# Optimization experiments

Hardware: AMD Instinct MI355X
Metric: run time of the kernel (lower is better)

## Reference

```python
import jax, jax.numpy as jnp
import numpy as np

N = 50000
E = 400000
IN_FEATS = 512
HEADS = 8
OUT_FEATS = 64
NEG_SLOPE = 0.2


def setup_inputs() -> dict:
    key = jax.random.key(0)
    ks = jax.random.split(key, 12)
    HF = HEADS * OUT_FEATS
    s = 1.0 / np.sqrt(IN_FEATS)
    inp = {
        "feat": jax.random.normal(ks[0], (N, IN_FEATS), dtype=jnp.float32),
        "src": jax.random.randint(ks[1], (E,), 0, N, dtype=jnp.int32),
        "dst": jax.random.randint(ks[2], (E,), 0, N, dtype=jnp.int32),
        "W_src": jax.random.normal(ks[3], (IN_FEATS, HF), dtype=jnp.float32) * s,
        "b_src": jax.random.normal(ks[4], (HF,), dtype=jnp.float32) * 0.01,
        "W_dst": jax.random.normal(ks[5], (IN_FEATS, HF), dtype=jnp.float32) * s,
        "b_dst": jax.random.normal(ks[6], (HF,), dtype=jnp.float32) * 0.01,
        "W_val": jax.random.normal(ks[7], (IN_FEATS, HF), dtype=jnp.float32) * s,
        "b_val": jax.random.normal(ks[8], (HF,), dtype=jnp.float32) * 0.01,
        "attn_l": jax.random.normal(ks[9], (HEADS, OUT_FEATS), dtype=jnp.float32) * 0.1,
        "attn_r": jax.random.normal(ks[10], (HEADS, OUT_FEATS), dtype=jnp.float32) * 0.1,
    }
    return inp


def reference(feat, src, dst, W_src, b_src, W_dst, b_dst, W_val, b_val, attn_l, attn_r):
    # node projections: [N, H, F]
    feat_src = (feat @ W_src + b_src).reshape(N, HEADS, OUT_FEATS)
    feat_dst = (feat @ W_dst + b_dst).reshape(N, HEADS, OUT_FEATS)
    feat_v = (feat @ W_val + b_val).reshape(N, HEADS, OUT_FEATS)

    # per-node attention logits: [N, H]
    el = jnp.einsum("nhf,hf->nh", feat_src, attn_l)
    er = jnp.einsum("nhf,hf->nh", feat_dst, attn_r)

    # per-edge logits with leaky relu: [E, H]
    e = el[src] + er[dst]
    e = jnp.where(e >= 0, e, NEG_SLOPE * e)

    # edge softmax segmented by destination node
    e_max = jax.ops.segment_max(e, dst, num_segments=N)  # [N, H]
    e_max = jnp.where(jnp.isfinite(e_max), e_max, 0.0)
    exp_e = jnp.exp(e - e_max[dst])  # [E, H]
    denom = jax.ops.segment_sum(exp_e, dst, num_segments=N)  # [N, H]
    a = exp_e / jnp.maximum(denom[dst], 1e-16)  # [E, H]

    # weighted gather-scatter aggregation: [N, H, F]
    msg = feat_v[src] * a[:, :, None]
    rst = jax.ops.segment_sum(msg, dst, num_segments=N)
    return rst.reshape(N, HEADS * OUT_FEATS)
```

## Files before the change

kernel.cpp:

```cpp
#include <hip/hip_runtime.h>
#include <math.h>

constexpr int N_NODES = 50000;
constexpr int N_PAD   = 50048;
constexpr int N_EDGES = 400000;
constexpr int IN_F = 512;
constexpr int HEADS = 8;
constexpr int OUT_F = 64;
constexpr int HF = 512;
constexpr float NEG = 0.2f;

typedef __bf16 bf16x8 __attribute__((ext_vector_type(8)));
typedef float  f32x4  __attribute__((ext_vector_type(4)));

__device__ __forceinline__ unsigned short f2bf(float f) {
    unsigned u = __float_as_uint(f);
    u += 0x7fffu + ((u >> 16) & 1u);
    return (unsigned short)(u >> 16);
}
__device__ __forceinline__ unsigned packbf2(float lo, float hi) {
    return (unsigned)f2bf(lo) | ((unsigned)f2bf(hi) << 16);
}

constexpr int K0_CONV_BLOCKS = 12500;
constexpr int K0_ZERO_BLOCKS = (N_NODES + 255) / 256;

__global__ __launch_bounds__(256) void k0_convert(const float* __restrict__ in,
                                                  unsigned short* __restrict__ out,
                                                  int* __restrict__ deg) {
    int b = blockIdx.x;
    if (b < K0_CONV_BLOCKS) {
        int idx = b * 256 + threadIdx.x;
        size_t base = (size_t)idx * 8;
        float4 a = *(const float4*)(in + base);
        float4 c = *(const float4*)(in + base + 4);
        uint4 v;
        v.x = packbf2(a.x, a.y);
        v.y = packbf2(a.z, a.w);
        v.z = packbf2(c.x, c.y);
        v.w = packbf2(c.z, c.w);
        *(uint4*)(out + base) = v;
    } else {
        int idx = (b - K0_CONV_BLOCKS) * 256 + threadIdx.x;
        if (idx < N_NODES) deg[idx] = 0;
    }
}

constexpr int K14_HIST0 = 289;
constexpr int K14_BLOCKS = K14_HIST0 + (N_EDGES + 255) / 256;

__global__ __launch_bounds__(256) void k14_misc(
        const float* __restrict__ W_val, unsigned short* __restrict__ Wt,
        const float* __restrict__ W_src, const float* __restrict__ b_src,
        const float* __restrict__ W_dst, const float* __restrict__ b_dst,
        const float* __restrict__ attn_l, const float* __restrict__ attn_r,
        float* __restrict__ w_l, float* __restrict__ w_r,
        float* __restrict__ c_l, float* __restrict__ c_r,
        const int* __restrict__ dst, int* __restrict__ deg) {
    __shared__ float tile[32][33];
    int b = blockIdx.x, t = threadIdx.x;
    if (b < 256) {
        int bi = b >> 4, bj = b & 15;
        for (int i = t; i < 1024; i += 256) {
            int r = i >> 5, c = i & 31;
            tile[r][c] = W_val[(size_t)(bi * 32 + r) * HF + bj * 32 + c];
        }
        __syncthreads();
        for (int i = t; i < 1024; i += 256) {
            int r = i >> 5, c = i & 31;
            Wt[(size_t)(bj * 32 + r) * IN_F + bi * 32 + c] = f2bf(tile[c][r]);
        }
    } else if (b < K14_HIST0) {
        int gid = (b - 256) * 256 + t;
        if (gid < 4096) {
            int k = gid >> 3, h = gid & 7;
            float s = 0.f;
            #pragma unroll 8
            for (int f = 0; f < OUT_F; ++f) s += W_src[k * HF + h * OUT_F + f] * attn_l[h * OUT_F + f];
            w_l[k * 8 + h] = s;
        } else if (gid < 8192) {
            int g = gid - 4096;
            int k = g >> 3, h = g & 7;
            float s = 0.f;
            #pragma unroll 8
            for (int f = 0; f < OUT_F; ++f) s += W_dst[k * HF + h * OUT_F + f] * attn_r[h * OUT_F + f];
            w_r[k * 8 + h] = s;
        } else if (gid < 8192 + 16) {
            int g = gid - 8192;
            int h = g & 7;
            float s = 0.f;
            if (g < 8) {
                for (int f = 0; f < OUT_F; ++f) s += b_src[h * OUT_F + f] * attn_l[h * OUT_F + f];
                c_l[h] = s;
            } else {
                for (int f = 0; f < OUT_F; ++f) s += b_dst[h * OUT_F + f] * attn_r[h * OUT_F + f];
                c_r[h] = s;
            }
        }
    } else {
        int e = (b - K14_HIST0) * 256 + t;
        if (e < N_EDGES) atomicAdd(&deg[dst[e]], 1);
    }
}

__global__ __launch_bounds__(256) void k2_el_er(
        const float* __restrict__ feat,
        const float* __restrict__ w_l, const float* __restrict__ w_r,
        const float* __restrict__ c_l, const float* __restrict__ c_r,
        float* __restrict__ el, float* __restrict__ er) {
    __shared__ float swl[4096];
    __shared__ float swr[4096];
    int t = threadIdx.x;
    for (int i = t; i < 4096; i += 256) { swl[i] = w_l[i]; swr[i] = w_r[i]; }
    __syncthreads();

    int node = blockIdx.x * 16 + (t >> 4);
    if (node >= N_NODES) return;
    int sub = t & 15, h = sub & 7, side = sub >> 3;

    const float* w = side ? swr : swl;
    float acc = side ? c_r[h] : c_l[h];
    const float* frow = feat + (size_t)node * IN_F;
    for (int k = 0; k < IN_F; k += 4) {
        float4 f = *(const float4*)(frow + k);
        acc = fmaf(f.x, w[(k + 0) * 8 + h], acc);
        acc = fmaf(f.y, w[(k + 1) * 8 + h], acc);
        acc = fmaf(f.z, w[(k + 2) * 8 + h], acc);
        acc = fmaf(f.w, w[(k + 3) * 8 + h], acc);
    }
    if (side) er[node * 8 + h] = acc; else el[node * 8 + h] = acc;
}

__global__ __launch_bounds__(1024) void kS_scan(const int* __restrict__ deg,
                                                int* __restrict__ offs,
                                                int* __restrict__ cursor) {
    __shared__ int wsum[16];
    __shared__ int base_s;
    int b = blockIdx.x, t = threadIdx.x;
    int lane = t & 63, wid = t >> 6;

    int pre = 0;
    for (int i = t; i < b * 1024; i += 1024) pre += deg[i];
    #pragma unroll
    for (int off = 32; off; off >>= 1) pre += __shfl_down(pre, (unsigned)off, 64);
    if (lane == 0) wsum[wid] = pre;
    __syncthreads();
    if (t == 0) {
        int s = 0;
        for (int i = 0; i < 16; ++i) s += wsum[i];
        base_s = s;
    }
    __syncthreads();
    int base = base_s;
    __syncthreads();

    int i = b * 1024 + t;
    int v = (i < N_NODES) ? deg[i] : 0;
    int x = v;
    #pragma unroll
    for (int off = 1; off < 64; off <<= 1) {
        int y = __shfl_up(x, (unsigned)off, 64);
        if (lane >= off) x += y;
    }
    if (lane == 63) wsum[wid] = x;
    __syncthreads();
    if (wid == 0) {
        int s = (lane < 16) ? wsum[lane] : 0;
        #pragma unroll
        for (int off = 1; off < 16; off <<= 1) {
            int y = __shfl_up(s, (unsigned)off, 64);
            if (lane >= off) s += y;
        }
        if (lane < 16) wsum[lane] = s;
    }
    __syncthreads();
    int woff = wid ? wsum[wid - 1] : 0;
    if (i < N_NODES) {
        int excl = base + woff + x - v;
        offs[i] = excl;
        cursor[i] = excl;
    }
}

__global__ __launch_bounds__(256) void k3_mfma(
        const unsigned short* __restrict__ Abf,
        const unsigned short* __restrict__ Bbf,
        const float* __restrict__ bias,
        unsigned short* __restrict__ C) {
    __shared__ unsigned short As[128 * 64];
    __shared__ unsigned short Bs[128 * 64];
    int tid = threadIdx.x;
    int w = tid >> 6, lane = tid & 63;
    int bm = blockIdx.x >> 2, bn = blockIdx.x & 3;
    int rowBase = bm * 128, colBase = bn * 128;
    int wm = w >> 1, wn = w & 1;
    int c15 = lane & 15, q = lane >> 4;

    f32x4 acc[4][4] = {};

    for (int k0 = 0; k0 < IN_F; k0 += 64) {
        #pragma unroll
        for (int rnd = 0; rnd < 4; ++rnd) {
            int e = w * 256 + rnd * 64 + lane;
            int r = e >> 3, p = e & 7;
            int lc = p ^ (r & 7);
            const unsigned short* gA = Abf + (size_t)(rowBase + r) * IN_F + k0 + lc * 8;
            unsigned short* lA = &As[(w * 256 + rnd * 64) * 8];
            __builtin_amdgcn_global_load_lds(
                (const __attribute__((address_space(1))) unsigned int*)gA,
                (__attribute__((address_space(3))) unsigned int*)lA, 16, 0, 0);
            const unsigned short* gB = Bbf + (size_t)(colBase + r) * IN_F + k0 + lc * 8;
            unsigned short* lB = &Bs[(w * 256 + rnd * 64) * 8];
            __builtin_amdgcn_global_load_lds(
                (const __attribute__((address_space(1))) unsigned int*)gB,
                (__attribute__((address_space(3))) unsigned int*)lB, 16, 0, 0);
        }
        __syncthreads();

        #pragma unroll
        for (int ks = 0; ks < 2; ++ks) {
            bf16x8 a[4], b[4];
            #pragma unroll
            for (int mi = 0; mi < 4; ++mi) {
                int row = wm * 64 + mi * 16 + c15;
                int pc = (ks * 4 + q) ^ (row & 7);
                a[mi] = *(const bf16x8*)&As[row * 64 + pc * 8];
            }
            #pragma unroll
            for (int nj = 0; nj < 4; ++nj) {
                int row = wn * 64 + nj * 16 + c15;
                int pc = (ks * 4 + q) ^ (row & 7);
                b[nj] = *(const bf16x8*)&Bs[row * 64 + pc * 8];
            }
            #pragma unroll
            for (int mi = 0; mi < 4; ++mi)
                #pragma unroll
                for (int nj = 0; nj < 4; ++nj)
                    acc[mi][nj] = __builtin_amdgcn_mfma_f32_16x16x32_bf16(
                        a[mi], b[nj], acc[mi][nj], 0, 0, 0);
        }
        __syncthreads();
    }

    #pragma unroll
    for (int nj = 0; nj < 4; ++nj) {
        int col = colBase + wn * 64 + nj * 16 + c15;
        float bv = bias[col];
        #pragma unroll
        for (int mi = 0; mi < 4; ++mi) {
            int row0 = rowBase + wm * 64 + mi * 16 + q * 4;
            #pragma unroll
            for (int rg = 0; rg < 4; ++rg) {
                C[(size_t)(row0 + rg) * HF + col] = f2bf(acc[mi][nj][rg] + bv);
            }
        }
    }
}

__global__ __launch_bounds__(256) void k6_scatter(
        const int* __restrict__ src, const int* __restrict__ dst,
        int* __restrict__ cursor, int* __restrict__ srcs) {
    int e = blockIdx.x * 256 + threadIdx.x;
    if (e < N_EDGES) {
        int pos = atomicAdd(&cursor[dst[e]], 1);
        srcs[pos] = src[e];
    }
}

__device__ __forceinline__ void accum8(float* acc, uint4 v, float w) {
    unsigned u;
    u = v.x;
    acc[0] = fmaf(w, __uint_as_float(u << 16), acc[0]);
    acc[1] = fmaf(w, __uint_as_float(u & 0xffff0000u), acc[1]);
    u = v.y;
    acc[2] = fmaf(w, __uint_as_float(u << 16), acc[2]);
    acc[3] = fmaf(w, __uint_as_float(u & 0xffff0000u), acc[3]);
    u = v.z;
    acc[4] = fmaf(w, __uint_as_float(u << 16), acc[4]);
    acc[5] = fmaf(w, __uint_as_float(u & 0xffff0000u), acc[5]);
    u = v.w;
    acc[6] = fmaf(w, __uint_as_float(u << 16), acc[6]);
    acc[7] = fmaf(w, __uint_as_float(u & 0xffff0000u), acc[7]);
}

__global__ __launch_bounds__(256) void k8_agg(
        const int* __restrict__ srcs, const int* __restrict__ offs,
        const int* __restrict__ deg,
        const float* __restrict__ el, const float* __restrict__ er,
        const uint4* __restrict__ feat_v,
        float* __restrict__ out) {
    int lane = threadIdx.x & 63;
    int n = blockIdx.x * 4 + (threadIdx.x >> 6);
    int start = offs[n], cnt = deg[n];
    int h = lane >> 3;
    float erh = er[(size_t)n * 8 + h];
    float acc[8] = {};
    float dsum = 0.f;

    for (int base = 0; base < cnt; base += 64) {
        int m = cnt - base; if (m > 64) m = 64;
        int s_all = (lane < m) ? srcs[start + base + lane] : 0;
        int i = 0;
        for (; i + 8 <= m; i += 8) {
            int s[8]; uint4 v[8]; float e[8];
            #pragma unroll
            for (int j = 0; j < 8; ++j) s[j] = __shfl(s_all, i + j, 64);
            #pragma unroll
            for (int j = 0; j < 8; ++j) v[j] = feat_v[(size_t)s[j] * 64 + lane];
            #pragma unroll
            for (int j = 0; j < 8; ++j) e[j] = el[(size_t)s[j] * 8 + h];
            #pragma unroll
            for (int j = 0; j < 8; ++j) {
                float x = e[j] + erh;
                x = (x >= 0.f) ? x : NEG * x;
                float w = __expf(x);
                dsum += w;
                accum8(acc, v[j], w);
            }
        }
        for (; i < m; ++i) {
            int s0 = __shfl(s_all, i, 64);
            uint4 v0 = feat_v[(size_t)s0 * 64 + lane];
            float x = el[(size_t)s0 * 8 + h] + erh;
            x = (x >= 0.f) ? x : NEG * x;
            float w = __expf(x);
            dsum += w;
            accum8(acc, v0, w);
        }
    }

    float dn = 1.f / fmaxf(dsum, 1e-16f);
    float* op = out + (size_t)n * HF + lane * 8;
    *(float4*)op       = make_float4(acc[0] * dn, acc[1] * dn, acc[2] * dn, acc[3] * dn);
    *(float4*)(op + 4) = make_float4(acc[4] * dn, acc[5] * dn, acc[6] * dn, acc[7] * dn);
}

extern "C" void kernel_launch(void* const* d_in, const int* in_sizes, int n_in,
                              void* d_out, int out_size, void* d_ws, size_t ws_size,
                              hipStream_t stream) {
    const float* feat   = (const float*)d_in[0];
    const int*   src    = (const int*)d_in[1];
    const int*   dst    = (const int*)d_in[2];
    const float* W_src  = (const float*)d_in[3];
    const float* b_src  = (const float*)d_in[4];
    const float* W_dst  = (const float*)d_in[5];
    const float* b_dst  = (const float*)d_in[6];
    const float* W_val  = (const float*)d_in[7];
    const float* b_val  = (const float*)d_in[8];
    const float* attn_l = (const float*)d_in[9];
    const float* attn_r = (const float*)d_in[10];
    float* out = (float*)d_out;

    char* ws = (char*)d_ws;
    size_t off = 0;
    auto alloc = [&](size_t bytes) -> void* {
        void* p = ws + off;
        off += (bytes + 255) & ~(size_t)255;
        return p;
    };

    unsigned short* feat_bf = (unsigned short*)alloc((size_t)N_PAD * IN_F * 2);
    unsigned short* Wt      = (unsigned short*)alloc((size_t)IN_F * HF * 2);
    unsigned short* feat_v  = (unsigned short*)alloc((size_t)N_PAD * HF * 2);
    float* w_l    = (float*)alloc(4096 * 4);
    float* w_r    = (float*)alloc(4096 * 4);
    float* c_l    = (float*)alloc(8 * 4);
    float* c_r    = (float*)alloc(8 * 4);
    float* el     = (float*)alloc((size_t)N_NODES * 8 * 4);
    float* er     = (float*)alloc((size_t)N_NODES * 8 * 4);
    int*   deg    = (int*)alloc((size_t)N_NODES * 4);
    int*   offs   = (int*)alloc((size_t)N_NODES * 4);
    int*   cursor = (int*)alloc((size_t)N_NODES * 4);
    int*   srcs   = (int*)alloc((size_t)N_EDGES * 4);
    (void)ws_size; (void)in_sizes; (void)n_in; (void)out_size;

    k0_convert<<<K0_CONV_BLOCKS + K0_ZERO_BLOCKS, 256, 0, stream>>>(feat, feat_bf, deg);
    k14_misc<<<K14_BLOCKS, 256, 0, stream>>>(W_val, Wt, W_src, b_src, W_dst, b_dst,
                                             attn_l, attn_r, w_l, w_r, c_l, c_r, dst, deg);
    k2_el_er<<<(N_NODES + 15) / 16, 256, 0, stream>>>(feat, w_l, w_r, c_l, c_r, el, er);
    kS_scan<<<(N_NODES + 1023) / 1024, 1024, 0, stream>>>(deg, offs, cursor);
    k3_mfma<<<(N_PAD / 128) * 4, 256, 0, stream>>>(feat_bf, Wt, b_val, feat_v);
    k6_scatter<<<(N_EDGES + 255) / 256, 256, 0, stream>>>(src, dst, cursor, srcs);
    k8_agg<<<N_NODES / 4, 256, 0, stream>>>(srcs, offs, deg, el, er,
                                            (const uint4*)feat_v, out);
}
```

Before: 422.9 us.

## Fuse bf16 feature conversion with el/er projection in persistent kernel

Merges the fp32-to-bf16 conversion of feat and the per-node el/er logit projection into one persistent kernel, so feat (about 100 MB) is read once instead of twice. Each wave handles one row, keeps its slice of the folded attention weights in registers, prefetches the next row, and reduces the 16 outputs with a transpose-style shuffle butterfly. Degree zeroing moves to hipMemsetAsync. The cost is heavy register use from 32 float4 weight registers, and a fixed grid of 1024 blocks.

```diff
diff --git a/kernel.cpp b/kernel.cpp
--- a/kernel.cpp
+++ b/kernel.cpp
@@ -20,30 +20,6 @@
 }
 __device__ __forceinline__ unsigned packbf2(float lo, float hi) {
     return (unsigned)f2bf(lo) | ((unsigned)f2bf(hi) << 16);
-}
-
-constexpr int K0_CONV_BLOCKS = 12500;
-constexpr int K0_ZERO_BLOCKS = (N_NODES + 255) / 256;
-
-__global__ __launch_bounds__(256) void k0_convert(const float* __restrict__ in,
-                                                  unsigned short* __restrict__ out,
-                                                  int* __restrict__ deg) {
-    int b = blockIdx.x;
-    if (b < K0_CONV_BLOCKS) {
-        int idx = b * 256 + threadIdx.x;
-        size_t base = (size_t)idx * 8;
-        float4 a = *(const float4*)(in + base);
-        float4 c = *(const float4*)(in + base + 4);
-        uint4 v;
-        v.x = packbf2(a.x, a.y);
-        v.y = packbf2(a.z, a.w);
-        v.z = packbf2(c.x, c.y);
-        v.w = packbf2(c.z, c.w);
-        *(uint4*)(out + base) = v;
-    } else {
-        int idx = (b - K0_CONV_BLOCKS) * 256 + threadIdx.x;
-        if (idx < N_NODES) deg[idx] = 0;
-    }
 }
 
 constexpr int K14_HIST0 = 289;
@@ -103,32 +79,137 @@
     }
 }
 
-__global__ __launch_bounds__(256) void k2_el_er(
+constexpr int K0F_GRID = 1024;
+
+__global__ __launch_bounds__(256, 2) void k0_fused(
         const float* __restrict__ feat,
         const float* __restrict__ w_l, const float* __restrict__ w_r,
         const float* __restrict__ c_l, const float* __restrict__ c_r,
+        unsigned short* __restrict__ feat_bf,
         float* __restrict__ el, float* __restrict__ er) {
-    __shared__ float swl[4096];
-    __shared__ float swr[4096];
+    __shared__ float4 lw[2048];
     int t = threadIdx.x;
-    for (int i = t; i < 4096; i += 256) { swl[i] = w_l[i]; swr[i] = w_r[i]; }
-    __syncthreads();
-
-    int node = blockIdx.x * 16 + (t >> 4);
-    if (node >= N_NODES) return;
-    int sub = t & 15, h = sub & 7, side = sub >> 3;
-
-    const float* w = side ? swr : swl;
-    float acc = side ? c_r[h] : c_l[h];
-    const float* frow = feat + (size_t)node * IN_F;
-    for (int k = 0; k < IN_F; k += 4) {
-        float4 f = *(const float4*)(frow + k);
-        acc = fmaf(f.x, w[(k + 0) * 8 + h], acc);
-        acc = fmaf(f.y, w[(k + 1) * 8 + h], acc);
-        acc = fmaf(f.z, w[(k + 2) * 8 + h], acc);
-        acc = fmaf(f.w, w[(k + 3) * 8 + h], acc);
-    }
-    if (side) er[node * 8 + h] = acc; else el[node * 8 + h] = acc;
+    int lane = t & 63, wv = t >> 6;
+
+    const float4* gl = (const float4*)w_l;
+    const float4* gr = (const float4*)w_r;
+    #pragma unroll
+    for (int p = 0; p < 8; ++p) {
+        int i = t + 256 * p;
+        int sw = i ^ ((i >> 4) & 7);
+        lw[sw] = (i < 1024) ? gl[i] : gr[i - 1024];
+    }
+    __syncthreads();
+
+    float4 wl0[8], wl1[8], wr0[8], wr1[8];
+    #pragma unroll
+    for (int j = 0; j < 8; ++j) {
+        int i0 = 16 * lane + 2 * j;
+        wl0[j] = lw[i0 ^ ((i0 >> 4) & 7)];
+        int i1 = i0 + 1;
+        wl1[j] = lw[i1 ^ ((i1 >> 4) & 7)];
+        int i2 = 1024 + i0;
+        wr0[j] = lw[i2 ^ ((i2 >> 4) & 7)];
+        int i3 = i2 + 1;
+        wr1[j] = lw[i3 ^ ((i3 >> 4) & 7)];
+    }
+
+    int idx = ((lane & 1) << 3) | ((lane & 2) << 1) | ((lane & 4) >> 1) | ((lane & 8) >> 3);
+    int oh = idx & 7, oside = idx >> 3;
+    float cadd = 0.f;
+    if (lane < 16) cadd = oside ? c_r[oh] : c_l[oh];
+
+    const int NQ = N_NODES / 4;
+    int q = blockIdx.x;
+    if (q >= NQ) return;
+
+    float4 f0, f1;
+    {
+        const float* fr = feat + (size_t)(q * 4 + wv) * IN_F + lane * 8;
+        f0 = *(const float4*)fr;
+        f1 = *(const float4*)(fr + 4);
+    }
+
+    while (true) {
+        int qn = q + K0F_GRID;
+        float4 n0, n1;
+        if (qn < NQ) {
+            const float* fr = feat + (size_t)(qn * 4 + wv) * IN_F + lane * 8;
+            n0 = *(const float4*)fr;
+            n1 = *(const float4*)(fr + 4);
+        }
+
+        int row = q * 4 + wv;
+        uint4 vv;
+        vv.x = packbf2(f0.x, f0.y); vv.y = packbf2(f0.z, f0.w);
+        vv.z = packbf2(f1.x, f1.y); vv.w = packbf2(f1.z, f1.w);
+        *(uint4*)(feat_bf + (size_t)row * IN_F + lane * 8) = vv;
+
+        float v[16];
+        #pragma unroll
+        for (int c = 0; c < 16; ++c) v[c] = 0.f;
+        float ff[8] = {f0.x, f0.y, f0.z, f0.w, f1.x, f1.y, f1.z, f1.w};
+        #pragma unroll
+        for (int j = 0; j < 8; ++j) {
+            float f = ff[j];
+            v[0]  = fmaf(f, wl0[j].x, v[0]);
+            v[1]  = fmaf(f, wl0[j].y, v[1]);
+            v[2]  = fmaf(f, wl0[j].z, v[2]);
+            v[3]  = fmaf(f, wl0[j].w, v[3]);
+            v[4]  = fmaf(f, wl1[j].x, v[4]);
+            v[5]  = fmaf(f, wl1[j].y, v[5]);
+            v[6]  = fmaf(f, wl1[j].z, v[6]);
+            v[7]  = fmaf(f, wl1[j].w, v[7]);
+            v[8]  = fmaf(f, wr0[j].x, v[8]);
+            v[9]  = fmaf(f, wr0[j].y, v[9]);
+            v[10] = fmaf(f, wr0[j].z, v[10]);
+            v[11] = fmaf(f, wr0[j].w, v[11]);
+            v[12] = fmaf(f, wr1[j].x, v[12]);
+            v[13] = fmaf(f, wr1[j].y, v[13]);
+            v[14] = fmaf(f, wr1[j].z, v[14]);
+            v[15] = fmaf(f, wr1[j].w, v[15]);
+        }
+
+        #pragma unroll
+        for (int j = 0; j < 8; ++j) {
+            float a = v[j], b = v[j + 8];
+            float send = (lane & 1) ? a : b;
+            float recv = __shfl_xor(send, 1, 64);
+            v[j] = ((lane & 1) ? b : a) + recv;
+        }
+        #pragma unroll
+        for (int j = 0; j < 4; ++j) {
+            float a = v[j], b = v[j + 4];
+            float send = (lane & 2) ? a : b;
+            float recv = __shfl_xor(send, 2, 64);
+            v[j] = ((lane & 2) ? b : a) + recv;
+        }
+        #pragma unroll
+        for (int j = 0; j < 2; ++j) {
+            float a = v[j], b = v[j + 2];
+            float send = (lane & 4) ? a : b;
+            float recv = __shfl_xor(send, 4, 64);
+            v[j] = ((lane & 4) ? b : a) + recv;
+        }
+        {
+            float a = v[0], b = v[1];
+            float send = (lane & 8) ? a : b;
+            float recv = __shfl_xor(send, 8, 64);
+            v[0] = ((lane & 8) ? b : a) + recv;
+        }
+        float tot = v[0];
+        tot += __shfl_xor(tot, 16, 64);
+        tot += __shfl_xor(tot, 32, 64);
+
+        if (lane < 16) {
+            float o = tot + cadd;
+            if (oside) er[(size_t)row * 8 + oh] = o;
+            else       el[(size_t)row * 8 + oh] = o;
+        }
+
+        if (qn >= NQ) break;
+        q = qn; f0 = n0; f1 = n1;
+    }
 }
 
 __global__ __launch_bounds__(1024) void kS_scan(const int* __restrict__ deg,
@@ -374,10 +455,10 @@
     int*   srcs   = (int*)alloc((size_t)N_EDGES * 4);
     (void)ws_size; (void)in_sizes; (void)n_in; (void)out_size;
 
-    k0_convert<<<K0_CONV_BLOCKS + K0_ZERO_BLOCKS, 256, 0, stream>>>(feat, feat_bf, deg);
+    hipMemsetAsync(deg, 0, (size_t)N_NODES * 4, stream);
     k14_misc<<<K14_BLOCKS, 256, 0, stream>>>(W_val, Wt, W_src, b_src, W_dst, b_dst,
                                              attn_l, attn_r, w_l, w_r, c_l, c_r, dst, deg);
-    k2_el_er<<<(N_NODES + 15) / 16, 256, 0, stream>>>(feat, w_l, w_r, c_l, c_r, el, er);
+    k0_fused<<<K0F_GRID, 256, 0, stream>>>(feat, w_l, w_r, c_l, c_r, feat_bf, el, er);
     kS_scan<<<(N_NODES + 1023) / 1024, 1024, 0, stream>>>(deg, offs, cursor);
     k3_mfma<<<(N_PAD / 128) * 4, 256, 0, stream>>>(feat_bf, Wt, b_val, feat_v);
     k6_scatter<<<(N_EDGES + 255) / 256, 256, 0, stream>>>(src, dst, cursor, srcs);
```

Result: faster. 377.5 us (-10.7%).

## Fuse fp32-to-bf16 conversion and el/er logits into the MFMA projection GEMM

Applied to the files above, without the earlier changes.

Removes the separate feature conversion kernel and the el/er dot-product kernel. The GEMM now loads fp32 features directly, converts them to bf16 into LDS, and computes the 16 per-node attention logits with extra MFMAs against a bf16 folded weight matrix in one column-block. This avoids writing and re-reading a bf16 copy of feat and a second full pass over feat. In exchange, A-tile loads become synchronous register loads instead of async global-to-LDS loads, and the logits are now computed in bf16 precision rather than fp32.

```diff
diff --git a/kernel.cpp b/kernel.cpp
--- a/kernel.cpp
+++ b/kernel.cpp
@@ -22,30 +22,6 @@
     return (unsigned)f2bf(lo) | ((unsigned)f2bf(hi) << 16);
 }
 
-constexpr int K0_CONV_BLOCKS = 12500;
-constexpr int K0_ZERO_BLOCKS = (N_NODES + 255) / 256;
-
-__global__ __launch_bounds__(256) void k0_convert(const float* __restrict__ in,
-                                                  unsigned short* __restrict__ out,
-                                                  int* __restrict__ deg) {
-    int b = blockIdx.x;
-    if (b < K0_CONV_BLOCKS) {
-        int idx = b * 256 + threadIdx.x;
-        size_t base = (size_t)idx * 8;
-        float4 a = *(const float4*)(in + base);
-        float4 c = *(const float4*)(in + base + 4);
-        uint4 v;
-        v.x = packbf2(a.x, a.y);
-        v.y = packbf2(a.z, a.w);
-        v.z = packbf2(c.x, c.y);
-        v.w = packbf2(c.z, c.w);
-        *(uint4*)(out + base) = v;
-    } else {
-        int idx = (b - K0_CONV_BLOCKS) * 256 + threadIdx.x;
-        if (idx < N_NODES) deg[idx] = 0;
-    }
-}
-
 constexpr int K14_HIST0 = 289;
 constexpr int K14_BLOCKS = K14_HIST0 + (N_EDGES + 255) / 256;
 
@@ -54,8 +30,7 @@
         const float* __restrict__ W_src, const float* __restrict__ b_src,
         const float* __restrict__ W_dst, const float* __restrict__ b_dst,
         const float* __restrict__ attn_l, const float* __restrict__ attn_r,
-        float* __restrict__ w_l, float* __restrict__ w_r,
-        float* __restrict__ c_l, float* __restrict__ c_r,
+        unsigned short* __restrict__ w_lr, float* __restrict__ c_lr,
         const int* __restrict__ dst, int* __restrict__ deg) {
     __shared__ float tile[32][33];
     int b = blockIdx.x, t = threadIdx.x;
@@ -77,58 +52,30 @@
             float s = 0.f;
             #pragma unroll 8
             for (int f = 0; f < OUT_F; ++f) s += W_src[k * HF + h * OUT_F + f] * attn_l[h * OUT_F + f];
-            w_l[k * 8 + h] = s;
+            w_lr[h * IN_F + k] = f2bf(s);
         } else if (gid < 8192) {
             int g = gid - 4096;
             int k = g >> 3, h = g & 7;
             float s = 0.f;
             #pragma unroll 8
             for (int f = 0; f < OUT_F; ++f) s += W_dst[k * HF + h * OUT_F + f] * attn_r[h * OUT_F + f];
-            w_r[k * 8 + h] = s;
+            w_lr[(8 + h) * IN_F + k] = f2bf(s);
         } else if (gid < 8192 + 16) {
             int g = gid - 8192;
             int h = g & 7;
             float s = 0.f;
             if (g < 8) {
                 for (int f = 0; f < OUT_F; ++f) s += b_src[h * OUT_F + f] * attn_l[h * OUT_F + f];
-                c_l[h] = s;
+                c_lr[h] = s;
             } else {
                 for (int f = 0; f < OUT_F; ++f) s += b_dst[h * OUT_F + f] * attn_r[h * OUT_F + f];
-                c_r[h] = s;
+                c_lr[8 + h] = s;
             }
         }
     } else {
         int e = (b - K14_HIST0) * 256 + t;
         if (e < N_EDGES) atomicAdd(&deg[dst[e]], 1);
     }
-}
-
-__global__ __launch_bounds__(256) void k2_el_er(
-        const float* __restrict__ feat,
-        const float* __restrict__ w_l, const float* __restrict__ w_r,
-        const float* __restrict__ c_l, const float* __restrict__ c_r,
-        float* __restrict__ el, float* __restrict__ er) {
-    __shared__ float swl[4096];
-    __shared__ float swr[4096];
-    int t = threadIdx.x;
-    for (int i = t; i < 4096; i += 256) { swl[i] = w_l[i]; swr[i] = w_r[i]; }
-    __syncthreads();
-
-    int node = blockIdx.x * 16 + (t >> 4);
-    if (node >= N_NODES) return;
-    int sub = t & 15, h = sub & 7, side = sub >> 3;
-
-    const float* w = side ? swr : swl;
-    float acc = side ? c_r[h] : c_l[h];
-    const float* frow = feat + (size_t)node * IN_F;
-    for (int k = 0; k < IN_F; k += 4) {
-        float4 f = *(const float4*)(frow + k);
-        acc = fmaf(f.x, w[(k + 0) * 8 + h], acc);
-        acc = fmaf(f.y, w[(k + 1) * 8 + h], acc);
-        acc = fmaf(f.z, w[(k + 2) * 8 + h], acc);
-        acc = fmaf(f.w, w[(k + 3) * 8 + h], acc);
-    }
-    if (side) er[node * 8 + h] = acc; else el[node * 8 + h] = acc;
 }
 
 __global__ __launch_bounds__(1024) void kS_scan(const int* __restrict__ deg,
@@ -182,11 +129,16 @@
     }
 }
 
-__global__ __launch_bounds__(256) void k3_mfma(
-        const unsigned short* __restrict__ Abf,
+constexpr int K3_GRID = (N_PAD / 128) * 4;
+
+__global__ __launch_bounds__(256) void k3_fused(
+        const float* __restrict__ feat,
         const unsigned short* __restrict__ Bbf,
+        const unsigned short* __restrict__ w_lr,
+        const float* __restrict__ c_lr,
         const float* __restrict__ bias,
-        unsigned short* __restrict__ C) {
+        unsigned short* __restrict__ C,
+        float* __restrict__ el, float* __restrict__ er) {
     __shared__ unsigned short As[128 * 64];
     __shared__ unsigned short Bs[128 * 64];
     int tid = threadIdx.x;
@@ -195,8 +147,10 @@
     int rowBase = bm * 128, colBase = bn * 128;
     int wm = w >> 1, wn = w & 1;
     int c15 = lane & 15, q = lane >> 4;
+    bool doE = (bn == 0) && (wn == 0);
 
     f32x4 acc[4][4] = {};
+    f32x4 accE[4] = {};
 
     for (int k0 = 0; k0 < IN_F; k0 += 64) {
         #pragma unroll
@@ -204,16 +158,26 @@
             int e = w * 256 + rnd * 64 + lane;
             int r = e >> 3, p = e & 7;
             int lc = p ^ (r & 7);
-            const unsigned short* gA = Abf + (size_t)(rowBase + r) * IN_F + k0 + lc * 8;
-            unsigned short* lA = &As[(w * 256 + rnd * 64) * 8];
-            __builtin_amdgcn_global_load_lds(
-                (const __attribute__((address_space(1))) unsigned int*)gA,
-                (__attribute__((address_space(3))) unsigned int*)lA, 16, 0, 0);
             const unsigned short* gB = Bbf + (size_t)(colBase + r) * IN_F + k0 + lc * 8;
-            unsigned short* lB = &Bs[(w * 256 + rnd * 64) * 8];
+            unsigned short* lB = &Bs[e * 8];
             __builtin_amdgcn_global_load_lds(
                 (const __attribute__((address_space(1))) unsigned int*)gB,
                 (__attribute__((address_space(3))) unsigned int*)lB, 16, 0, 0);
+        }
+        #pragma unroll
+        for (int rnd = 0; rnd < 4; ++rnd) {
+            int e = w * 256 + rnd * 64 + lane;
+            int r = e >> 3, p = e & 7;
+            int lc = p ^ (r & 7);
+            int row = rowBase + r;
+            if (row > N_NODES - 1) row = N_NODES - 1;
+            const float* gA = feat + (size_t)row * IN_F + k0 + lc * 8;
+            float4 fa = *(const float4*)gA;
+            float4 fb = *(const float4*)(gA + 4);
+            uint4 pk;
+            pk.x = packbf2(fa.x, fa.y); pk.y = packbf2(fa.z, fa.w);
+            pk.z = packbf2(fb.x, fb.y); pk.w = packbf2(fb.z, fb.w);
+            *(uint4*)&As[e * 8] = pk;
         }
         __syncthreads();
 
@@ -238,6 +202,13 @@
                 for (int nj = 0; nj < 4; ++nj)
                     acc[mi][nj] = __builtin_amdgcn_mfma_f32_16x16x32_bf16(
                         a[mi], b[nj], acc[mi][nj], 0, 0, 0);
+            if (doE) {
+                bf16x8 be = *(const bf16x8*)(w_lr + (size_t)c15 * IN_F + k0 + ks * 32 + q * 8);
+                #pragma unroll
+                for (int mi = 0; mi < 4; ++mi)
+                    accE[mi] = __builtin_amdgcn_mfma_f32_16x16x32_bf16(
+                        a[mi], be, accE[mi], 0, 0, 0);
+            }
         }
         __syncthreads();
     }
@@ -252,6 +223,21 @@
             #pragma unroll
             for (int rg = 0; rg < 4; ++rg) {
                 C[(size_t)(row0 + rg) * HF + col] = f2bf(acc[mi][nj][rg] + bv);
+            }
+        }
+    }
+
+    if (doE) {
+        float cadd = c_lr[c15];
+        int side = c15 >> 3, hh = c15 & 7;
+        #pragma unroll
+        for (int mi = 0; mi < 4; ++mi) {
+            int row0 = rowBase + wm * 64 + mi * 16 + q * 4;
+            #pragma unroll
+            for (int rg = 0; rg < 4; ++rg) {
+                float v = accE[mi][rg] + cadd;
+                if (side) er[(size_t)(row0 + rg) * 8 + hh] = v;
+                else      el[(size_t)(row0 + rg) * 8 + hh] = v;
             }
         }
     }
@@ -359,27 +345,24 @@
         return p;
     };
 
-    unsigned short* feat_bf = (unsigned short*)alloc((size_t)N_PAD * IN_F * 2);
     unsigned short* Wt      = (unsigned short*)alloc((size_t)IN_F * HF * 2);
     unsigned short* feat_v  = (unsigned short*)alloc((size_t)N_PAD * HF * 2);
-    float* w_l    = (float*)alloc(4096 * 4);
-    float* w_r    = (float*)alloc(4096 * 4);
-    float* c_l    = (float*)alloc(8 * 4);
-    float* c_r    = (float*)alloc(8 * 4);
-    float* el     = (float*)alloc((size_t)N_NODES * 8 * 4);
-    float* er     = (float*)alloc((size_t)N_NODES * 8 * 4);
+    unsigned short* w_lr    = (unsigned short*)alloc((size_t)16 * IN_F * 2);
+    float* c_lr   = (float*)alloc(16 * 4);
+    float* el     = (float*)alloc((size_t)N_PAD * 8 * 4);
+    float* er     = (float*)alloc((size_t)N_PAD * 8 * 4);
     int*   deg    = (int*)alloc((size_t)N_NODES * 4);
     int*   offs   = (int*)alloc((size_t)N_NODES * 4);
     int*   cursor = (int*)alloc((size_t)N_NODES * 4);
     int*   srcs   = (int*)alloc((size_t)N_EDGES * 4);
     (void)ws_size; (void)in_sizes; (void)n_in; (void)out_size;
 
-    k0_convert<<<K0_CONV_BLOCKS + K0_ZERO_BLOCKS, 256, 0, stream>>>(feat, feat_bf, deg);
+    hipMemsetAsync(deg, 0, (size_t)N_NODES * 4, stream);
     k14_misc<<<K14_BLOCKS, 256, 0, stream>>>(W_val, Wt, W_src, b_src, W_dst, b_dst,
-                                             attn_l, attn_r, w_l, w_r, c_l, c_r, dst, deg);
-    k2_el_er<<<(N_NODES + 15) / 16, 256, 0, stream>>>(feat, w_l, w_r, c_l, c_r, el, er);
+                                             attn_l, attn_r, w_lr, c_lr, dst, deg);
     kS_scan<<<(N_NODES + 1023) / 1024, 1024, 0, stream>>>(deg, offs, cursor);
-    k3_mfma<<<(N_PAD / 128) * 4, 256, 0, stream>>>(feat_bf, Wt, b_val, feat_v);
+    k3_fused<<<K3_GRID, 256, 0, stream>>>(feat, Wt, w_lr, c_lr, b_val,
+                                          feat_v, el, er);
     k6_scatter<<<(N_EDGES + 255) / 256, 256, 0, stream>>>(src, dst, cursor, srcs);
     k8_agg<<<N_NODES / 4, 256, 0, stream>>>(srcs, offs, deg, el, er,
                                             (const uint4*)feat_v, out);
```

Result: faster. 369.1 us (-12.7%).
